# Optimization experiments

Measured on AMD Instinct MI355X. Metric: run time of the kernel, lower is better.

Reference implementation:

```python
import jax, jax.numpy as jnp
import numpy as np

N = 8192   # supervoxels in current scan (queries: mean_features / ori_coords)
M = 8192   # surrounding supervoxels (keys: sur_sv_feature / sur_sv_coords)
C = 96     # feature channels
OUT = 20   # semantic classes
LG = 2048  # number of labeled supervoxels


def _pairwise_l2(x, y):
    # squared euclidean distances [n, m], clamped at 0 like torch.clamp(d, 0, inf)
    xn = jnp.sum(x * x, axis=1)[:, None]
    yn = jnp.sum(y * y, axis=1)[None, :]
    d = xn + yn - 2.0 * (x @ y.T)
    return jnp.maximum(d, 0.0)


def _cosine_distance(x1, x2, eps=1e-8):
    w1 = jnp.linalg.norm(x1, axis=1, keepdims=True)
    w2 = jnp.linalg.norm(x2, axis=1, keepdims=True)
    return 1.0 - (x1 @ x2.T) / jnp.maximum(w1 * w2.T, eps)


def setup_inputs() -> dict:
    key = jax.random.key(0)
    ks = jax.random.split(key, 8)
    sur_sv_feature = 0.05 * jax.random.normal(ks[0], (M, C), jnp.float32)
    sur_sv_coords = 0.3 * jax.random.normal(ks[1], (M, 3), jnp.float32)
    gt_idx = jax.random.randint(ks[2], (M,), 0, OUT)
    sur_sv_gt = jnp.eye(OUT, dtype=jnp.float32)[gt_idx]
    sv_prob = jax.random.normal(ks[3], (N, OUT), jnp.float32)
    mean_features = 0.05 * jax.random.normal(ks[4], (N, C), jnp.float32)
    ori_coords = 0.3 * jax.random.normal(ks[5], (N, 3), jnp.float32)
    # two near-identity invertible 4x4 pose matrices
    posses = jnp.eye(4, dtype=jnp.float32)[None, :, :] + 0.02 * jax.random.normal(ks[6], (2, 4, 4), jnp.float32)
    ran_mask = jax.random.randint(ks[7], (M,), 0, 20).astype(jnp.int32)  # torch.randint(20, ...)
    return dict(sur_sv_feature=sur_sv_feature, sur_sv_coords=sur_sv_coords,
                sur_sv_gt=sur_sv_gt, sv_prob=sv_prob, mean_features=mean_features,
                ori_coords=ori_coords, posses=posses, ran_mask=ran_mask, lg=LG)


def reference(sur_sv_feature, sur_sv_coords, sur_sv_gt, sv_prob,
              mean_features, ori_coords, posses, ran_mask, lg):
    # branch: rev=1, idx=0, sf=None
    sv_prob_sm = jax.nn.softmax(sv_prob, axis=1)
    ori_coords_in = ori_coords
    # alginment: diff = inv(posses[1]) @ posses[0]; homogeneous transform
    diff = jnp.linalg.inv(posses[1]) @ posses[0]
    homog = jnp.concatenate([sur_sv_coords,
                             jnp.ones((sur_sv_coords.shape[0], 1), sur_sv_coords.dtype)], axis=1)
    al_sur_sv_coords = (homog @ diff.T)[:, :3]

    feat_dist_cos = _cosine_distance(mean_features, sur_sv_feature)          # [N, M]
    coords_dist = _pairwise_l2(ori_coords_in, al_sur_sv_coords) / 0.25       # / 0.5**2
    sim = (1.0 + feat_dist_cos - jnp.exp(-0.5 * coords_dist)).T              # [M, N]
    sm_index = jnp.argmin(sim, axis=1)                                       # [M] nearest query per key

    onehot = sur_sv_gt
    mid_feat = mean_features[sm_index]       # [M, C]
    mid_coord = ori_coords_in[sm_index]      # [M, 3]

    upd = jnp.argmax(onehot, axis=1) < 9
    upd = upd.at[:lg].set(True)
    upd = jnp.logical_or(upd, ran_mask == 1)                                 # random refresh mask

    # masked (instead of gathered) weighted label propagation: zeroed columns
    # contribute nothing to either numerator or denominator -> same math as
    # index-selecting the update columns.
    fd = _pairwise_l2(mean_features, mid_feat)                               # [N, M]
    cd = _pairwise_l2(ori_coords_in, mid_coord) / 0.25
    dist_matric = jnp.exp(-0.5 * cd / 0.25 - 0.5 * fd / 0.09) * upd[None, :].astype(fd.dtype)
    uw = (dist_matric @ onehot) / (jnp.sum(dist_matric, axis=1, keepdims=True) + 1e-16)

    sv_prob_updated = 0.5 * sv_prob_sm + 0.5 * uw

    # re-inject labeled gt where the propagated prob agrees enough
    tmpx = jnp.argmax(onehot[:lg], axis=1)                                   # [lg]
    idx_lg = sm_index[:lg]
    vals = sv_prob_updated[idx_lg, tmpx]
    tmp = vals > 0.1
    tmp = jnp.where(jnp.any(tmp), tmp, vals > 0.0)                           # fallback threshold
    new_rows = jnp.where(tmp[:, None], onehot[:lg], sv_prob_updated[idx_lg])
    sv_prob_updated = sv_prob_updated.at[idx_lg].set(new_rows)

    maxv = jnp.max(sv_prob_updated, axis=1)
    trust9 = maxv >= 0.9
    trust = jnp.where(jnp.any(trust9), trust9, maxv >= 0.85)                 # [N] bool mask (padded form of torch.nonzero)
    pre = jnp.eye(OUT, dtype=sv_prob_updated.dtype)[jnp.argmax(sv_prob_updated, axis=1)]

    m = trust[:, None].astype(mean_features.dtype)
    return (trust, mean_features * m, ori_coords * m, pre * m,
            uw, sv_prob_updated, sm_index)
```

## Files before the change

kernel.cpp:

```cpp
#include <hip/hip_runtime.h>
#include <math.h>

#define N 8192
#define M 8192
#define C 96
#define OUT 20
#define LG 2048

#define KP2 192
#define NSPA 4
#define NSPB 4

typedef _Float16 h8 __attribute__((ext_vector_type(8)));
typedef float    f4 __attribute__((ext_vector_type(4)));

__device__ __forceinline__ void gl_lds16(const h8* g, h8* l) {
    __builtin_amdgcn_global_load_lds(
        (const __attribute__((address_space(1))) unsigned int*)g,
        (__attribute__((address_space(3))) unsigned int*)l,
        16, 0, 0);
}

__device__ __forceinline__ size_t tsm24(int row, int slot) {
    return ((size_t)(row >> 7) * 24 + slot) * 128 + (row & 127);
}

constexpr size_t OFF_DIFF  = 0;
constexpr size_t OFF_AL    = 256;
constexpr size_t OFF_UPDF  = OFF_AL    + (size_t)M*3*4;
constexpr size_t OFF_GTC   = OFF_UPDF  + (size_t)M*4;
constexpr size_t OFF_SMI   = OFF_GTC   + (size_t)M*4;
constexpr size_t OFF_PERM  = OFF_SMI   + (size_t)M*4;
constexpr size_t OFF_AP    = OFF_PERM  + (size_t)M*4;
constexpr size_t OFF_BQ    = OFF_AP    + (size_t)M*KP2*2;
constexpr size_t OFF_MFP   = OFF_BQ    + (size_t)N*KP2*2;
constexpr size_t OFF_MIDQ  = OFF_MFP   + (size_t)N*KP2*2;
constexpr size_t OFF_PAV   = OFF_MIDQ  + (size_t)(M+256)*KP2*2;
constexpr size_t OFF_PAI   = OFF_PAV   + (size_t)NSPA*M*4;
constexpr size_t OFF_PB    = OFF_PAI   + (size_t)NSPA*M*4;
constexpr size_t OFF_VALS  = OFF_PB    + (size_t)NSPB*N*OUT*4;
constexpr size_t OFF_POS   = OFF_VALS  + (size_t)LG*4;
constexpr size_t OFF_MAXV  = OFF_POS   + (size_t)N*4;
constexpr size_t OFF_AMAX  = OFF_MAXV  + (size_t)N*4;
constexpr size_t OFF_FLAGS = OFF_AMAX  + (size_t)N*4;
constexpr size_t OFF_CNT   = OFF_FLAGS + 256;
constexpr size_t OFF_META  = OFF_CNT   + 256;
constexpr size_t OFF_NQ4   = OFF_META  + 256;
constexpr size_t OFF_SIDEQ = OFF_NQ4   + (size_t)N*16;
constexpr size_t OFF_SIDEC = OFF_SIDEQ + (size_t)(M+256)*16;

__global__ void k_diff(const float* __restrict__ posses, float* __restrict__ diff) {
    if (threadIdx.x != 0 || blockIdx.x != 0) return;
    float a[4][8];
    for (int i = 0; i < 4; i++)
        for (int j = 0; j < 4; j++) {
            a[i][j]     = posses[16 + i*4 + j];
            a[i][4 + j] = (i == j) ? 1.f : 0.f;
        }
    for (int col = 0; col < 4; col++) {
        int piv = col; float mx = fabsf(a[col][col]);
        for (int r = col + 1; r < 4; r++) {
            float v = fabsf(a[r][col]);
            if (v > mx) { mx = v; piv = r; }
        }
        if (piv != col)
            for (int j = 0; j < 8; j++) { float t = a[col][j]; a[col][j] = a[piv][j]; a[piv][j] = t; }
        float inv = 1.0f / a[col][col];
        for (int j = 0; j < 8; j++) a[col][j] *= inv;
        for (int r = 0; r < 4; r++) {
            if (r == col) continue;
            float f = a[r][col];
            for (int j = 0; j < 8; j++) a[r][j] -= f * a[col][j];
        }
    }
    for (int i = 0; i < 4; i++)
        for (int j = 0; j < 4; j++) {
            float s = 0.f;
            for (int k = 0; k < 4; k++) s += a[i][4 + k] * posses[k*4 + j];
            diff[i*4 + j] = s;
        }
}

__global__ void k_prep_m(const float* __restrict__ ssf, const float* __restrict__ scoords,
                         const float* __restrict__ gt, const int* __restrict__ ran_mask,
                         const float* __restrict__ diff,
                         float* __restrict__ al, _Float16* __restrict__ aP,
                         float* __restrict__ updf, int* __restrict__ gtcls,
                         int* __restrict__ cnt) {
    __shared__ int hcnt[OUT];
    const int tt = threadIdx.x;
    if (tt < OUT) hcnt[tt] = 0;
    __syncthreads();
    const int m = blockIdx.x * 32 + (tt >> 1);
    const int h = tt & 1;
    {
        const float4* r4 = (const float4*)(ssf + (size_t)m * C);
        float4 row[12]; float s = 0.f;
        #pragma unroll
        for (int c = 0; c < 12; c++) {
            float4 v = r4[h*12 + c];
            row[c] = v;
            s += v.x*v.x + v.y*v.y + v.z*v.z + v.w*v.w;
        }
        s += __shfl_xor(s, 1, 64);
        float scale = 256.0f / sqrtf(s);
        h8* dst = (h8*)aP;
        #pragma unroll
        for (int qq = 0; qq < 6; qq++) {
            int q = h*6 + qq;
            float4 u = row[2*qq], v = row[2*qq+1];
            float xs[8] = {u.x,u.y,u.z,u.w,v.x,v.y,v.z,v.w};
            h8 hi, lo;
            #pragma unroll
            for (int e = 0; e < 8; e++) {
                float xv = xs[e] * scale;
                _Float16 hh = (_Float16)xv;
                hi[e] = hh;
                lo[e] = (_Float16)(xv - (float)hh);
            }
            dst[tsm24(m, q)]      = hi;
            dst[tsm24(m, 12 + q)] = lo;
        }
        if (h == 0) {
            float x = scoords[m*3], y = scoords[m*3+1], z = scoords[m*3+2];
            #pragma unroll
            for (int j = 0; j < 3; j++)
                al[m*3 + j] = diff[j*4+0]*x + diff[j*4+1]*y + diff[j*4+2]*z + diff[j*4+3];
            int best = 0; float bv = gt[(size_t)m*OUT];
            #pragma unroll
            for (int k = 1; k < OUT; k++) {
                float v = gt[(size_t)m*OUT + k];
                if (v > bv) { bv = v; best = k; }
            }
            gtcls[m] = best;
            bool upd = (best < 9 || m < LG || ran_mask[m] == 1);
            updf[m] = upd ? 1.f : 0.f;
            if (upd) atomicAdd(&hcnt[best], 1);
        }
    }
    __syncthreads();
    if (tt < OUT) atomicAdd(&cnt[tt], hcnt[tt]);
}

__global__ void k_prep_n(const float* __restrict__ mf, const float* __restrict__ ori,
                         _Float16* __restrict__ bQ, _Float16* __restrict__ mfP,
                         float4* __restrict__ nq4) {
    const int tt = threadIdx.x;
    const int n = blockIdx.x * 32 + (tt >> 1);
    const int h = tt & 1;
    const float4* r4 = (const float4*)(mf + (size_t)n * C);
    float4 row[12]; float s = 0.f;
    #pragma unroll
    for (int c = 0; c < 12; c++) {
        float4 v = r4[h*12 + c];
        row[c] = v;
        s += v.x*v.x + v.y*v.y + v.z*v.z + v.w*v.w;
    }
    s += __shfl_xor(s, 1, 64);
    if (h == 0) {
        float4 o;
        o.x = ori[n*3]; o.y = ori[n*3+1]; o.z = ori[n*3+2]; o.w = s;
        nq4[n] = o;
    }
    float scn = 256.0f / sqrtf(s);
    h8* dB = (h8*)bQ;
    h8* dF = (h8*)mfP;
    #pragma unroll
    for (int qq = 0; qq < 6; qq++) {
        int q = h*6 + qq;
        float4 u = row[2*qq], v = row[2*qq+1];
        float xs[8] = {u.x,u.y,u.z,u.w,v.x,v.y,v.z,v.w};
        h8 hiN, loN, hiF, loF;
        #pragma unroll
        for (int e = 0; e < 8; e++) {
            float xn = xs[e] * scn;
            _Float16 hn = (_Float16)xn;
            hiN[e] = hn; loN[e] = (_Float16)(xn - (float)hn);
            float xf = xs[e] * 256.0f;
            _Float16 hf = (_Float16)xf;
            hiF[e] = hf; loF[e] = (_Float16)(xf - (float)hf);
        }
        dB[tsm24(n, q)]    = hiN;
        dB[tsm24(n, 12+q)] = loN;
        dF[tsm24(n, q)]    = hiF;
        dF[tsm24(n, 12+q)] = loF;
    }
}

__global__ __launch_bounds__(1024, 1) void k_argmin(
        const _Float16* __restrict__ aP, const _Float16* __restrict__ bQ,
        const float* __restrict__ al, const float4* __restrict__ nq4,
        float* __restrict__ pav, int* __restrict__ pai) {
    __shared__ h8 sA[24*128];
    __shared__ h8 sB[2*24*128];
    __shared__ float xv[4*128];
    __shared__ int   xi[4*128];
    __shared__ float4 sMs[128];
    const int t = threadIdx.x;
    const int wave = t >> 6, lane = t & 63;
    const int col = lane & 15, quad = lane >> 4;
    const int wm = wave >> 2, wn = wave & 3;
    const int m0 = blockIdx.x * 128;
    const int sp = blockIdx.y;

    {
        const h8* gA = (const h8*)aP + (size_t)blockIdx.x * 3072;
        #pragma unroll
        for (int q = 0; q < 3; q++) gl_lds16(gA + q*1024 + t, sA + q*1024 + t);
    }
    if (t < 128) {
        float ax = al[(m0+t)*3+0], ay = al[(m0+t)*3+1], az = al[(m0+t)*3+2];
        sMs[t] = (float4){4.0f*ax, 4.0f*ay, 4.0f*az, -2.0f*(ax*ax+ay*ay+az*az)};
    }
    float best[8]; int bidx[8];
    #pragma unroll
    for (int e = 0; e < 8; e++) { best[e] = 3.4e38f; bidx[e] = 0; }

    const h8* gB = (const h8*)bQ;
    f4 acc[2][4];
    for (int u = 0; u < 32/NSPA; u++) {
        const int tile = sp + u*NSPA;
        __syncthreads();
        {
            const h8* g = gB + (size_t)(2*tile) * 3072;
            #pragma unroll
            for (int q = 0; q < 6; q++) gl_lds16(g + q*1024 + t, sB + q*1024 + t);
        }
        __syncthreads();
        #pragma unroll
        for (int i = 0; i < 2; i++)
            #pragma unroll
            for (int j = 0; j < 4; j++) acc[i][j] = (f4){0.f,0.f,0.f,0.f};

        #pragma unroll
        for (int ks = 0; ks < 3; ks++) {
            const int hs = ks*4 + quad;
            h8 ah[2], alo[2], bh[4], blo[4];
            #pragma unroll
            for (int i = 0; i < 2; i++) {
                int ml = wm*32 + i*16 + col;
                ah[i]  = sA[hs*128 + ml];
                alo[i] = sA[(12+hs)*128 + ml];
            }
            #pragma unroll
            for (int j = 0; j < 4; j++) {
                int r = wn*64 + j*16 + col;
                int tb = (r >> 7) * 3072, rl = r & 127;
                bh[j]  = sB[tb + hs*128 + rl];
                blo[j] = sB[tb + (12+hs)*128 + rl];
            }
            #pragma unroll
            for (int i = 0; i < 2; i++)
                #pragma unroll
                for (int j = 0; j < 4; j++) {
                    acc[i][j] = __builtin_amdgcn_mfma_f32_16x16x32_f16(ah[i],  bh[j],  acc[i][j], 0, 0, 0);
                    acc[i][j] = __builtin_amdgcn_mfma_f32_16x16x32_f16(ah[i],  blo[j], acc[i][j], 0, 0, 0);
                    acc[i][j] = __builtin_amdgcn_mfma_f32_16x16x32_f16(alo[i], bh[j],  acc[i][j], 0, 0, 0);
                }
        }
        const int n0t = tile * 256;
        float4 o4[4]; float bn[4]; int nidx[4];
        #pragma unroll
        for (int j = 0; j < 4; j++) {
            nidx[j] = n0t + wn*64 + j*16 + col;
            o4[j] = nq4[nidx[j]];
            bn[j] = -2.0f*(o4[j].x*o4[j].x + o4[j].y*o4[j].y + o4[j].z*o4[j].z);
        }
        #pragma unroll
        for (int e = 0; e < 8; e++) {
            int ml = wm*32 + (e>>2)*16 + quad*4 + (e&3);
            float4 sm = sMs[ml];
            #pragma unroll
            for (int j = 0; j < 4; j++) {
                float dot = acc[e>>2][j][e&3];
                float c = sm.w + bn[j];
                c = fmaf(sm.z, o4[j].z, c);
                c = fmaf(sm.y, o4[j].y, c);
                c = fmaf(sm.x, o4[j].x, c);
                float sim = fmaf(dot, -(1.0f/65536.0f), 2.0f) - __expf(c);
                if (sim < best[e]) { best[e] = sim; bidx[e] = nidx[j]; }
            }
        }
    }
    #pragma unroll
    for (int e = 0; e < 8; e++) {
        float bv = best[e]; int bi = bidx[e];
        #pragma unroll
        for (int d = 1; d < 16; d <<= 1) {
            float ov = __shfl_xor(bv, d, 64);
            int   oi = __shfl_xor(bi, d, 64);
            if (ov < bv || (ov == bv && oi < bi)) { bv = ov; bi = oi; }
        }
        best[e] = bv; bidx[e] = bi;
    }
    if (col == 0) {
        #pragma unroll
        for (int e = 0; e < 8; e++) {
            int ml = wm*32 + (e>>2)*16 + quad*4 + (e&3);
            xv[wn*128 + ml] = best[e];
            xi[wn*128 + ml] = bidx[e];
        }
    }
    __syncthreads();
    if (t < 128) {
        float bv = xv[t]; int bi = xi[t];
        #pragma unroll
        for (int w = 1; w < 4; w++) {
            float v = xv[w*128 + t]; int i2 = xi[w*128 + t];
            if (v < bv || (v == bv && i2 < bi)) { bv = v; bi = i2; }
        }
        pav[(size_t)sp * M + m0 + t] = bv;
        pai[(size_t)sp * M + m0 + t] = bi;
    }
}

__global__ void k_argmin_reduce(const float* __restrict__ pav, const int* __restrict__ pai,
                                int* __restrict__ smi, float* __restrict__ out_smi) {
    int m = blockIdx.x * 256 + threadIdx.x;
    if (m >= M) return;
    float best = 3.4e38f; int bidx = 0;
    for (int sp = 0; sp < NSPA; sp++) {
        float v = pav[(size_t)sp * M + m];
        int   i = pai[(size_t)sp * M + m];
        if (v < best || (v == best && i < bidx)) { best = v; bidx = i; }
    }
    smi[m] = bidx;
    out_smi[m] = (float)bidx;
}

__global__ void k_scan(const int* __restrict__ cnt, int* __restrict__ meta) {
    if (threadIdx.x != 0 || blockIdx.x != 0) return;
    int run = 0;
    for (int k = 0; k < OUT; k++) { meta[2 + k] = run; run += cnt[k]; }
    meta[0] = run;
    meta[1] = (run + 255) / 256;
}

__global__ void k_permute(const int* __restrict__ gtcls, const float* __restrict__ updf,
                          int* __restrict__ meta, int* __restrict__ perm) {
    int m = blockIdx.x * 256 + threadIdx.x;
    if (m >= M) return;
    if (updf[m] == 0.f) return;
    int pos = atomicAdd(&meta[2 + gtcls[m]], 1);
    perm[pos] = m;
}

__global__ void k_gather_sorted(const int* __restrict__ meta, const int* __restrict__ perm,
                                const int* __restrict__ smi, const int* __restrict__ gtcls,
                                const _Float16* __restrict__ mfP, const float4* __restrict__ nq4,
                                _Float16* __restrict__ midQ,
                                float4* __restrict__ sideQ, int* __restrict__ sideC) {
    int tid = blockIdx.x * 256 + threadIdx.x;
    int rr = tid / 24;
    int q  = tid - rr * 24;
    int mact = meta[0];
    int mpad = meta[1] * 256;
    if (rr >= mpad) return;
    h8* dst = (h8*)midQ;
    if (rr < mact) {
        int m = perm[rr];
        int s = smi[m];
        dst[tsm24(rr, q)] = ((const h8*)mfP)[tsm24(s, q)];
        if (q == 0) {
            float4 o = nq4[s];
            float4 sq;
            sq.x = o.w;
            sq.y = o.x; sq.z = o.y; sq.w = o.z;
            sideQ[rr] = sq;
            sideC[rr] = gtcls[m];
        }
    } else {
        dst[tsm24(rr, q)] = (h8)(_Float16)0.f;
        if (q == 0) {
            sideQ[rr] = (float4){1e9f, 0.f, 0.f, 0.f};
            sideC[rr] = 0;
        }
    }
}

__global__ __launch_bounds__(1024, 1) void k_uw(
        const _Float16* __restrict__ mfP, const _Float16* __restrict__ midQ,
        const float4* __restrict__ nq4,
        const float4* __restrict__ sideQ, const int* __restrict__ sideC,
        const int* __restrict__ meta, float* __restrict__ pb) {
    __shared__ h8 sN[24*128];
    __shared__ h8 sB[2*24*128];
    __shared__ float bins[128*21];
    __shared__ float4 sSa[128];
    __shared__ float  sSb[128];
    const int t = threadIdx.x;
    const int wave = t >> 6, lane = t & 63;
    const int col = lane & 15, quad = lane >> 4;
    const int wm = wave >> 2, wn = wave & 3;
    const int n0 = blockIdx.x * 128;
    const int sp = blockIdx.y;
    const int nmac = meta[1];

    {
        const h8* gN = (const h8*)mfP + (size_t)blockIdx.x * 3072;
        #pragma unroll
        for (int q = 0; q < 3; q++) gl_lds16(gN + q*1024 + t, sN + q*1024 + t);
    }
    if (t < 128) {
        float4 q = nq4[n0 + t];
        sSa[t] = (float4){q.x, q.y, q.z, -8.0f*(q.x*q.x + q.y*q.y + q.z*q.z)};
        sSb[t] = q.w;
    }
    for (int i = t; i < 128*21; i += 1024) bins[i] = 0.f;

    const h8* gB = (const h8*)midQ;
    f4 acc[2][4];
    for (int mt = sp; mt < nmac; mt += NSPB) {
        const int mb = mt * 256;
        __syncthreads();
        {
            const h8* g = gB + (size_t)(2*mt) * 3072;
            #pragma unroll
            for (int q = 0; q < 6; q++) gl_lds16(g + q*1024 + t, sB + q*1024 + t);
        }
        __syncthreads();
        #pragma unroll
        for (int i = 0; i < 2; i++)
            #pragma unroll
            for (int j = 0; j < 4; j++) acc[i][j] = (f4){0.f,0.f,0.f,0.f};

        #pragma unroll
        for (int ks = 0; ks < 3; ks++) {
            const int hs = ks*4 + quad;
            h8 ah[2], alo[2], bh[4], blo[4];
            #pragma unroll
            for (int i = 0; i < 2; i++) {
                int ml = wm*32 + i*16 + col;
                ah[i]  = sN[hs*128 + ml];
                alo[i] = sN[(12+hs)*128 + ml];
            }
            #pragma unroll
            for (int j = 0; j < 4; j++) {
                int r = wn*64 + j*16 + col;
                int tb = (r >> 7) * 3072, rl = r & 127;
                bh[j]  = sB[tb + hs*128 + rl];
                blo[j] = sB[tb + (12+hs)*128 + rl];
            }
            #pragma unroll
            for (int i = 0; i < 2; i++)
                #pragma unroll
                for (int j = 0; j < 4; j++) {
                    acc[i][j] = __builtin_amdgcn_mfma_f32_16x16x32_f16(ah[i],  bh[j],  acc[i][j], 0, 0, 0);
                    acc[i][j] = __builtin_amdgcn_mfma_f32_16x16x32_f16(ah[i],  blo[j], acc[i][j], 0, 0, 0);
                    acc[i][j] = __builtin_amdgcn_mfma_f32_16x16x32_f16(alo[i], bh[j],  acc[i][j], 0, 0, 0);
                }
        }
        {
            float m2[4], mx16[4], my16[4], mz16[4], bm[4]; int pc[4];
            #pragma unroll
            for (int j = 0; j < 4; j++) {
                int mm = mb + wn*64 + j*16 + col;
                float4 sq = sideQ[mm];
                m2[j] = sq.x;
                mx16[j] = 16.0f*sq.y; my16[j] = 16.0f*sq.z; mz16[j] = 16.0f*sq.w;
                bm[j] = -8.0f*(sq.y*sq.y + sq.z*sq.z + sq.w*sq.w);
                pc[j] = sideC[mm];
            }
            int seg0 = sideC[mb + wn*64];
            int seg1 = sideC[mb + wn*64 + 63];
            if (seg0 == seg1) {
                #pragma unroll
                for (int e = 0; e < 8; e++) {
                    int nl = wm*32 + (e>>2)*16 + quad*4 + (e&3);
                    float4 sa = sSa[nl];
                    float nn = sSb[nl];
                    float rs = 0.f;
                    #pragma unroll
                    for (int j = 0; j < 4; j++) {
                        float dot = acc[e>>2][j][e&3];
                        float tt = fmaf(dot, -2.0f*(1.0f/65536.0f), nn + m2[j]);
                        float fd = fmaxf(tt, 0.0f);
                        float c = sa.w + bm[j];
                        c = fmaf(sa.z, mz16[j], c);
                        c = fmaf(sa.y, my16[j], c);
                        c = fmaf(sa.x, mx16[j], c);
                        rs += __expf(fmaf(fd, -(0.5f/0.09f), c));
                    }
                    rs += __shfl_xor(rs, 1, 64);
                    rs += __shfl_xor(rs, 2, 64);
                    rs += __shfl_xor(rs, 4, 64);
                    rs += __shfl_xor(rs, 8, 64);
                    if (col == 0) atomicAdd(&bins[nl*21 + seg0], rs);
                }
            } else {
                #pragma unroll
                for (int e = 0; e < 8; e++) {
                    int nl = wm*32 + (e>>2)*16 + quad*4 + (e&3);
                    float4 sa = sSa[nl];
                    float nn = sSb[nl];
                    float cur = 0.f; int cc = -1;
                    #pragma unroll
                    for (int j = 0; j < 4; j++) {
                        float dot = acc[e>>2][j][e&3];
                        float tt = fmaf(dot, -2.0f*(1.0f/65536.0f), nn + m2[j]);
                        float fd = fmaxf(tt, 0.0f);
                        float c = sa.w + bm[j];
                        c = fmaf(sa.z, mz16[j], c);
                        c = fmaf(sa.y, my16[j], c);
                        c = fmaf(sa.x, mx16[j], c);
                        float w = __expf(fmaf(fd, -(0.5f/0.09f), c));
                        if (pc[j] != cc) {
                            if (cc >= 0) atomicAdd(&bins[nl*21 + cc], cur);
                            cc = pc[j]; cur = 0.f;
                        }
                        cur += w;
                    }
                    if (cc >= 0) atomicAdd(&bins[nl*21 + cc], cur);
                }
            }
        }
    }
    __syncthreads();
    for (int i = t; i < 128*OUT; i += 1024) {
        int loc = i / OUT, k = i - loc*OUT;
        pb[((size_t)sp*N + n0 + loc)*OUT + k] = bins[loc*21 + k];
    }
}

__global__ void k_uw_final(const float* __restrict__ pb, const float* __restrict__ svp,
                           float* __restrict__ out_uw, float* __restrict__ out_spu) {
    int n = blockIdx.x * 256 + threadIdx.x;
    if (n >= N) return;
    float s[OUT];
    #pragma unroll
    for (int k = 0; k < OUT; k++) s[k] = 0.f;
    for (int sp = 0; sp < NSPB; sp++) {
        size_t base = ((size_t)sp * N + n) * OUT;
        #pragma unroll
        for (int k = 0; k < OUT; k++) s[k] += pb[base + k];
    }
    float tot = 0.f;
    #pragma unroll
    for (int k = 0; k < OUT; k++) tot += s[k];
    float rden = 1.0f / (tot + 1e-16f);
    float p[OUT]; float mx = -3.4e38f;
    #pragma unroll
    for (int k = 0; k < OUT; k++) { p[k] = svp[(size_t)n*OUT + k]; mx = fmaxf(mx, p[k]); }
    float es = 0.f;
    #pragma unroll
    for (int k = 0; k < OUT; k++) { p[k] = __expf(p[k] - mx); es += p[k]; }
    float res = 1.0f / es;
    #pragma unroll
    for (int k = 0; k < OUT; k++) {
        float uw = s[k] * rden;
        out_uw[(size_t)n*OUT + k] = uw;
        out_spu[(size_t)n*OUT + k] = 0.5f * (p[k] * res) + 0.5f * uw;
    }
}

__global__ void k_scatter_pre(const int* __restrict__ smi, const int* __restrict__ gtcls,
                              const float* __restrict__ spu, float* __restrict__ vals,
                              int* __restrict__ pos, int* __restrict__ flags) {
    int i = blockIdx.x * 256 + threadIdx.x;
    if (i >= LG) return;
    int idx = smi[i];
    float v = spu[(size_t)idx*OUT + gtcls[i]];
    vals[i] = v;
    if (v > 0.1f) atomicOr(&flags[0], 1);
    atomicMax(&pos[idx], i);
}

__global__ void k_scatter_apply(const int* __restrict__ smi, const int* __restrict__ gtcls,
                                const float* __restrict__ vals, const int* __restrict__ pos,
                                const int* __restrict__ flags, float* __restrict__ spu) {
    int i = blockIdx.x * 256 + threadIdx.x;
    if (i >= LG) return;
    int idx = smi[i];
    if (pos[idx] != i) return;
    float v = vals[i];
    bool tmp = flags[0] ? (v > 0.1f) : (v > 0.0f);
    if (!tmp) return;
    int cls = gtcls[i];
    #pragma unroll
    for (int k = 0; k < OUT; k++) spu[(size_t)idx*OUT + k] = (k == cls) ? 1.0f : 0.0f;
}

__global__ void k_trust_pre(const float* __restrict__ spu, float* __restrict__ maxv,
                            int* __restrict__ amax, int* __restrict__ flags) {
    int n = blockIdx.x * 256 + threadIdx.x;
    if (n >= N) return;
    float best = spu[(size_t)n*OUT]; int bi = 0;
    #pragma unroll
    for (int k = 1; k < OUT; k++) {
        float v = spu[(size_t)n*OUT + k];
        if (v > best) { best = v; bi = k; }
    }
    maxv[n] = best; amax[n] = bi;
    if (best >= 0.9f) atomicOr(&flags[1], 1);
}

__global__ void k_finalize(const float* __restrict__ mf, const float* __restrict__ ori,
                           const float* __restrict__ maxv, const int* __restrict__ amax,
                           const int* __restrict__ flags,
                           float* __restrict__ out_trust, float* __restrict__ out_mf,
                           float* __restrict__ out_ori, float* __restrict__ out_pre) {
    int n = blockIdx.x * 256 + threadIdx.x;
    if (n >= N) return;
    float mv = maxv[n];
    bool tr = flags[1] ? (mv >= 0.9f) : (mv >= 0.85f);
    float m = tr ? 1.f : 0.f;
    out_trust[n] = m;
    const float4* src = (const float4*)(mf + (size_t)n * C);
    float4* dst = (float4*)(out_mf + (size_t)n * C);
    #pragma unroll
    for (int c = 0; c < 24; c++) {
        float4 v = src[c];
        v.x *= m; v.y *= m; v.z *= m; v.w *= m;
        dst[c] = v;
    }
    out_ori[n*3]   = ori[n*3]   * m;
    out_ori[n*3+1] = ori[n*3+1] * m;
    out_ori[n*3+2] = ori[n*3+2] * m;
    int bi = amax[n];
    #pragma unroll
    for (int k = 0; k < OUT; k++) out_pre[(size_t)n*OUT + k] = (k == bi) ? m : 0.f;
}

extern "C" void kernel_launch(void* const* d_in, const int* in_sizes, int n_in,
                              void* d_out, int out_size, void* d_ws, size_t ws_size,
                              hipStream_t stream) {
    (void)in_sizes; (void)n_in; (void)out_size; (void)ws_size;
    const float* ssf     = (const float*)d_in[0];
    const float* scoords = (const float*)d_in[1];
    const float* gt      = (const float*)d_in[2];
    const float* svp     = (const float*)d_in[3];
    const float* mf      = (const float*)d_in[4];
    const float* ori     = (const float*)d_in[5];
    const float* posses  = (const float*)d_in[6];
    const int*   ran     = (const int*)d_in[7];

    float* out = (float*)d_out;
    float* out_trust = out;
    float* out_mf    = out_trust + N;
    float* out_ori   = out_mf + (size_t)N*C;
    float* out_pre   = out_ori + (size_t)N*3;
    float* out_uw    = out_pre + (size_t)N*OUT;
    float* out_spu   = out_uw  + (size_t)N*OUT;
    float* out_smi   = out_spu + (size_t)N*OUT;

    char* ws = (char*)d_ws;
    float*     w_diff  = (float*)(ws + OFF_DIFF);
    float*     w_al    = (float*)(ws + OFF_AL);
    float*     w_updf  = (float*)(ws + OFF_UPDF);
    int*       w_gtc   = (int*)(ws + OFF_GTC);
    int*       w_smi   = (int*)(ws + OFF_SMI);
    int*       w_perm  = (int*)(ws + OFF_PERM);
    _Float16*  w_aP    = (_Float16*)(ws + OFF_AP);
    _Float16*  w_bQ    = (_Float16*)(ws + OFF_BQ);
    _Float16*  w_mfP   = (_Float16*)(ws + OFF_MFP);
    _Float16*  w_midQ  = (_Float16*)(ws + OFF_MIDQ);
    float*     w_pav   = (float*)(ws + OFF_PAV);
    int*       w_pai   = (int*)(ws + OFF_PAI);
    float*     w_pb    = (float*)(ws + OFF_PB);
    float*     w_vals  = (float*)(ws + OFF_VALS);
    int*       w_pos   = (int*)(ws + OFF_POS);
    float*     w_maxv  = (float*)(ws + OFF_MAXV);
    int*       w_amax  = (int*)(ws + OFF_AMAX);
    int*       w_flags = (int*)(ws + OFF_FLAGS);
    int*       w_cnt   = (int*)(ws + OFF_CNT);
    int*       w_meta  = (int*)(ws + OFF_META);
    float4*    w_nq4   = (float4*)(ws + OFF_NQ4);
    float4*    w_sideQ = (float4*)(ws + OFF_SIDEQ);
    int*       w_sideC = (int*)(ws + OFF_SIDEC);

    hipMemsetAsync(w_pos, 0xFF, (size_t)N*4, stream);
    hipMemsetAsync(w_flags, 0, 8, stream);
    hipMemsetAsync(w_cnt, 0, OUT*4, stream);

    k_diff<<<1, 64, 0, stream>>>(posses, w_diff);
    k_prep_m<<<M/32, 64, 0, stream>>>(ssf, scoords, gt, ran, w_diff,
                                      w_al, w_aP, w_updf, w_gtc, w_cnt);
    k_prep_n<<<N/32, 64, 0, stream>>>(mf, ori, w_bQ, w_mfP, w_nq4);
    k_argmin<<<dim3(M/128, NSPA), 1024, 0, stream>>>(w_aP, w_bQ, w_al, w_nq4, w_pav, w_pai);
    k_argmin_reduce<<<M/256, 256, 0, stream>>>(w_pav, w_pai, w_smi, out_smi);
    k_scan<<<1, 64, 0, stream>>>(w_cnt, w_meta);
    k_permute<<<M/256, 256, 0, stream>>>(w_gtc, w_updf, w_meta, w_perm);
    k_gather_sorted<<<((M+256)*24)/256, 256, 0, stream>>>(w_meta, w_perm, w_smi, w_gtc,
                                                          w_mfP, w_nq4,
                                                          w_midQ, w_sideQ, w_sideC);
    k_uw<<<dim3(N/128, NSPB), 1024, 0, stream>>>(w_mfP, w_midQ, w_nq4,
                                                 w_sideQ, w_sideC, w_meta, w_pb);
    k_uw_final<<<N/256, 256, 0, stream>>>(w_pb, svp, out_uw, out_spu);
    k_scatter_pre<<<LG/256, 256, 0, stream>>>(w_smi, w_gtc, out_spu, w_vals, w_pos, w_flags);
    k_scatter_apply<<<LG/256, 256, 0, stream>>>(w_smi, w_gtc, w_vals, w_pos, w_flags, out_spu);
    k_trust_pre<<<N/256, 256, 0, stream>>>(out_spu, w_maxv, w_amax, w_flags);
    k_finalize<<<N/256, 256, 0, stream>>>(mf, ori, w_maxv, w_amax, w_flags,
                                          out_trust, out_mf, out_ori, out_pre);
}
```

Baseline: 253.9 us.

## Double-buffer key tiles, drop low-half B operand, use shuffle-reduced class bins

The key matrix (midH) is now stored as the high fp16 half only, which halves gather and LDS traffic and removes one of the three MFMAs per split-precision product. Key tiles are prefetched into a second LDS buffer while the current one is being computed, so there is one barrier per iteration instead of two. The per-lane running class-segment atomics are replaced by a loop over classes with a cross-lane shuffle reduction and a single atomic per class. Dropping the low correction term on the key side lowers precision of the feature dot product, and the loop over classes may cost extra work when a tile spans several classes.

Result: faster. 228.3 us (-10.1%).

```diff
diff --git a/kernel.cpp b/kernel.cpp
--- a/kernel.cpp
+++ b/kernel.cpp
@@ -34,8 +34,8 @@
 constexpr size_t OFF_AP    = OFF_PERM  + (size_t)M*4;
 constexpr size_t OFF_BQ    = OFF_AP    + (size_t)M*KP2*2;
 constexpr size_t OFF_MFP   = OFF_BQ    + (size_t)N*KP2*2;
-constexpr size_t OFF_MIDQ  = OFF_MFP   + (size_t)N*KP2*2;
-constexpr size_t OFF_PAV   = OFF_MIDQ  + (size_t)(M+256)*KP2*2;
+constexpr size_t OFF_MIDH  = OFF_MFP   + (size_t)N*KP2*2;
+constexpr size_t OFF_PAV   = OFF_MIDH  + (size_t)(M+256)*192;
 constexpr size_t OFF_PAI   = OFF_PAV   + (size_t)NSPA*M*4;
 constexpr size_t OFF_PB    = OFF_PAI   + (size_t)NSPA*M*4;
 constexpr size_t OFF_VALS  = OFF_PB    + (size_t)NSPB*N*OUT*4;
@@ -348,19 +348,20 @@
 __global__ void k_gather_sorted(const int* __restrict__ meta, const int* __restrict__ perm,
                                 const int* __restrict__ smi, const int* __restrict__ gtcls,
                                 const _Float16* __restrict__ mfP, const float4* __restrict__ nq4,
-                                _Float16* __restrict__ midQ,
+                                _Float16* __restrict__ midH,
                                 float4* __restrict__ sideQ, int* __restrict__ sideC) {
     int tid = blockIdx.x * 256 + threadIdx.x;
-    int rr = tid / 24;
-    int q  = tid - rr * 24;
+    int rr = tid / 12;
+    int q  = tid - rr * 12;
     int mact = meta[0];
     int mpad = meta[1] * 256;
     if (rr >= mpad) return;
-    h8* dst = (h8*)midQ;
+    h8* dst = (h8*)midH;
+    size_t didx = ((size_t)(rr >> 7) * 12 + q) * 128 + (rr & 127);
     if (rr < mact) {
         int m = perm[rr];
         int s = smi[m];
-        dst[tsm24(rr, q)] = ((const h8*)mfP)[tsm24(s, q)];
+        dst[didx] = ((const h8*)mfP)[tsm24(s, q)];
         if (q == 0) {
             float4 o = nq4[s];
             float4 sq;
@@ -370,7 +371,7 @@
             sideC[rr] = gtcls[m];
         }
     } else {
-        dst[tsm24(rr, q)] = (h8)(_Float16)0.f;
+        dst[didx] = (h8)(_Float16)0.f;
         if (q == 0) {
             sideQ[rr] = (float4){1e9f, 0.f, 0.f, 0.f};
             sideC[rr] = 0;
@@ -379,12 +380,12 @@
 }
 
 __global__ __launch_bounds__(1024, 1) void k_uw(
-        const _Float16* __restrict__ mfP, const _Float16* __restrict__ midQ,
+        const _Float16* __restrict__ mfP, const _Float16* __restrict__ midH,
         const float4* __restrict__ nq4,
         const float4* __restrict__ sideQ, const int* __restrict__ sideC,
         const int* __restrict__ meta, float* __restrict__ pb) {
     __shared__ h8 sN[24*128];
-    __shared__ h8 sB[2*24*128];
+    __shared__ h8 sB[2][2*12*128];
     __shared__ float bins[128*21];
     __shared__ float4 sSa[128];
     __shared__ float  sSb[128];
@@ -400,6 +401,11 @@
         const h8* gN = (const h8*)mfP + (size_t)blockIdx.x * 3072;
         #pragma unroll
         for (int q = 0; q < 3; q++) gl_lds16(gN + q*1024 + t, sN + q*1024 + t);
+        if (sp < nmac) {
+            const h8* g = (const h8*)midH + (size_t)(2*sp) * 1536;
+            #pragma unroll
+            for (int q = 0; q < 3; q++) gl_lds16(g + q*1024 + t, sB[0] + q*1024 + t);
+        }
     }
     if (t < 128) {
         float4 q = nq4[n0 + t];
@@ -408,26 +414,27 @@
     }
     for (int i = t; i < 128*21; i += 1024) bins[i] = 0.f;
 
-    const h8* gB = (const h8*)midQ;
+    __syncthreads();
+
+    int cur = 0;
     f4 acc[2][4];
     for (int mt = sp; mt < nmac; mt += NSPB) {
         const int mb = mt * 256;
-        __syncthreads();
-        {
-            const h8* g = gB + (size_t)(2*mt) * 3072;
-            #pragma unroll
-            for (int q = 0; q < 6; q++) gl_lds16(g + q*1024 + t, sB + q*1024 + t);
-        }
-        __syncthreads();
+        if (mt + NSPB < nmac) {
+            const h8* g = (const h8*)midH + (size_t)(2*(mt + NSPB)) * 1536;
+            #pragma unroll
+            for (int q = 0; q < 3; q++) gl_lds16(g + q*1024 + t, sB[cur^1] + q*1024 + t);
+        }
         #pragma unroll
         for (int i = 0; i < 2; i++)
             #pragma unroll
             for (int j = 0; j < 4; j++) acc[i][j] = (f4){0.f,0.f,0.f,0.f};
 
+        const h8* sBc = sB[cur];
         #pragma unroll
         for (int ks = 0; ks < 3; ks++) {
             const int hs = ks*4 + quad;
-            h8 ah[2], alo[2], bh[4], blo[4];
+            h8 ah[2], alo[2], bh[4];
             #pragma unroll
             for (int i = 0; i < 2; i++) {
                 int ml = wm*32 + i*16 + col;
@@ -437,17 +444,15 @@
             #pragma unroll
             for (int j = 0; j < 4; j++) {
                 int r = wn*64 + j*16 + col;
-                int tb = (r >> 7) * 3072, rl = r & 127;
-                bh[j]  = sB[tb + hs*128 + rl];
-                blo[j] = sB[tb + (12+hs)*128 + rl];
+                int tb = (r >> 7) * 1536, rl = r & 127;
+                bh[j]  = sBc[tb + hs*128 + rl];
             }
             #pragma unroll
             for (int i = 0; i < 2; i++)
                 #pragma unroll
                 for (int j = 0; j < 4; j++) {
-                    acc[i][j] = __builtin_amdgcn_mfma_f32_16x16x32_f16(ah[i],  bh[j],  acc[i][j], 0, 0, 0);
-                    acc[i][j] = __builtin_amdgcn_mfma_f32_16x16x32_f16(ah[i],  blo[j], acc[i][j], 0, 0, 0);
-                    acc[i][j] = __builtin_amdgcn_mfma_f32_16x16x32_f16(alo[i], bh[j],  acc[i][j], 0, 0, 0);
+                    acc[i][j] = __builtin_amdgcn_mfma_f32_16x16x32_f16(ah[i],  bh[j], acc[i][j], 0, 0, 0);
+                    acc[i][j] = __builtin_amdgcn_mfma_f32_16x16x32_f16(alo[i], bh[j], acc[i][j], 0, 0, 0);
                 }
         }
         {
@@ -493,7 +498,7 @@
                     int nl = wm*32 + (e>>2)*16 + quad*4 + (e&3);
                     float4 sa = sSa[nl];
                     float nn = sSb[nl];
-                    float cur = 0.f; int cc = -1;
+                    float w[4];
                     #pragma unroll
                     for (int j = 0; j < 4; j++) {
                         float dot = acc[e>>2][j][e&3];
@@ -503,17 +508,23 @@
                         c = fmaf(sa.z, mz16[j], c);
                         c = fmaf(sa.y, my16[j], c);
                         c = fmaf(sa.x, mx16[j], c);
-                        float w = __expf(fmaf(fd, -(0.5f/0.09f), c));
-                        if (pc[j] != cc) {
-                            if (cc >= 0) atomicAdd(&bins[nl*21 + cc], cur);
-                            cc = pc[j]; cur = 0.f;
-                        }
-                        cur += w;
+                        w[j] = __expf(fmaf(fd, -(0.5f/0.09f), c));
                     }
-                    if (cc >= 0) atomicAdd(&bins[nl*21 + cc], cur);
+                    for (int cc = seg0; cc <= seg1; cc++) {
+                        float rs = 0.f;
+                        #pragma unroll
+                        for (int j = 0; j < 4; j++) rs += (pc[j] == cc) ? w[j] : 0.f;
+                        rs += __shfl_xor(rs, 1, 64);
+                        rs += __shfl_xor(rs, 2, 64);
+                        rs += __shfl_xor(rs, 4, 64);
+                        rs += __shfl_xor(rs, 8, 64);
+                        if (col == 0) atomicAdd(&bins[nl*21 + cc], rs);
+                    }
                 }
             }
         }
+        __syncthreads();
+        cur ^= 1;
     }
     __syncthreads();
     for (int i = t; i < 128*OUT; i += 1024) {
@@ -653,7 +664,7 @@
     _Float16*  w_aP    = (_Float16*)(ws + OFF_AP);
     _Float16*  w_bQ    = (_Float16*)(ws + OFF_BQ);
     _Float16*  w_mfP   = (_Float16*)(ws + OFF_MFP);
-    _Float16*  w_midQ  = (_Float16*)(ws + OFF_MIDQ);
+    _Float16*  w_midH  = (_Float16*)(ws + OFF_MIDH);
     float*     w_pav   = (float*)(ws + OFF_PAV);
     int*       w_pai   = (int*)(ws + OFF_PAI);
     float*     w_pb    = (float*)(ws + OFF_PB);
@@ -680,10 +691,10 @@
     k_argmin_reduce<<<M/256, 256, 0, stream>>>(w_pav, w_pai, w_smi, out_smi);
     k_scan<<<1, 64, 0, stream>>>(w_cnt, w_meta);
     k_permute<<<M/256, 256, 0, stream>>>(w_gtc, w_updf, w_meta, w_perm);
-    k_gather_sorted<<<((M+256)*24)/256, 256, 0, stream>>>(w_meta, w_perm, w_smi, w_gtc,
+    k_gather_sorted<<<((M+256)*12)/256, 256, 0, stream>>>(w_meta, w_perm, w_smi, w_gtc,
                                                           w_mfP, w_nq4,
-                                                          w_midQ, w_sideQ, w_sideC);
-    k_uw<<<dim3(N/128, NSPB), 1024, 0, stream>>>(w_mfP, w_midQ, w_nq4,
+                                                          w_midH, w_sideQ, w_sideC);
+    k_uw<<<dim3(N/128, NSPB), 1024, 0, stream>>>(w_mfP, w_midH, w_nq4,
                                                  w_sideQ, w_sideC, w_meta, w_pb);
     k_uw_final<<<N/256, 256, 0, stream>>>(w_pb, svp, out_uw, out_spu);
     k_scatter_pre<<<LG/256, 256, 0, stream>>>(w_smi, w_gtc, out_spu, w_vals, w_pos, w_flags);
```

## Double-buffer B tiles with async LDS prefetch and fold log2e into exp2

Applied to the files above, without the earlier changes.

In both the argmin and uw kernels, the 256-column B tile is halved to 128 columns, so it fits a ping-pong pair of LDS buffers. The next tile is prefetched via global_load_lds while the current one is computed, and each iteration needs one barrier instead of two. Exponentials become exp2f with LOG2E folded into the precomputed coefficients. The mixed-segment path in k_uw now reduces per class with wave shuffles plus one atomic per lane group, instead of per-lane atomics. Halving the tile gives each wave less MFMA work per barrier, and correctness depends on the async LDS writes having finished before the end-of-iteration barrier.

Result: no change. 249.1 us (-1.9%).

```diff
diff --git a/kernel.cpp b/kernel.cpp
--- a/kernel.cpp
+++ b/kernel.cpp
@@ -10,6 +10,7 @@
 #define KP2 192
 #define NSPA 4
 #define NSPB 4
+#define LOG2E 1.4426950408889634f
 
 typedef _Float16 h8 __attribute__((ext_vector_type(8)));
 typedef float    f4 __attribute__((ext_vector_type(4)));
@@ -192,7 +193,7 @@
         const float* __restrict__ al, const float4* __restrict__ nq4,
         float* __restrict__ pav, int* __restrict__ pai) {
     __shared__ h8 sA[24*128];
-    __shared__ h8 sB[2*24*128];
+    __shared__ h8 sB[2][24*128];
     __shared__ float xv[4*128];
     __shared__ int   xi[4*128];
     __shared__ float4 sMs[128];
@@ -207,35 +208,41 @@
         const h8* gA = (const h8*)aP + (size_t)blockIdx.x * 3072;
         #pragma unroll
         for (int q = 0; q < 3; q++) gl_lds16(gA + q*1024 + t, sA + q*1024 + t);
+        const h8* g = (const h8*)bQ + (size_t)sp * 3072;
+        #pragma unroll
+        for (int q = 0; q < 3; q++) gl_lds16(g + q*1024 + t, sB[0] + q*1024 + t);
     }
     if (t < 128) {
         float ax = al[(m0+t)*3+0], ay = al[(m0+t)*3+1], az = al[(m0+t)*3+2];
-        sMs[t] = (float4){4.0f*ax, 4.0f*ay, 4.0f*az, -2.0f*(ax*ax+ay*ay+az*az)};
+        sMs[t] = (float4){4.0f*LOG2E*ax, 4.0f*LOG2E*ay, 4.0f*LOG2E*az,
+                          -2.0f*LOG2E*(ax*ax+ay*ay+az*az)};
     }
     float best[8]; int bidx[8];
     #pragma unroll
     for (int e = 0; e < 8; e++) { best[e] = 3.4e38f; bidx[e] = 0; }
 
-    const h8* gB = (const h8*)bQ;
-    f4 acc[2][4];
-    for (int u = 0; u < 32/NSPA; u++) {
+    __syncthreads();
+
+    const int NT = (N/128) / NSPA;
+    int cur = 0;
+    f4 acc[2][2];
+    for (int u = 0; u < NT; u++) {
         const int tile = sp + u*NSPA;
-        __syncthreads();
-        {
-            const h8* g = gB + (size_t)(2*tile) * 3072;
-            #pragma unroll
-            for (int q = 0; q < 6; q++) gl_lds16(g + q*1024 + t, sB + q*1024 + t);
-        }
-        __syncthreads();
+        if (u + 1 < NT) {
+            const h8* g = (const h8*)bQ + (size_t)(sp + (u+1)*NSPA) * 3072;
+            #pragma unroll
+            for (int q = 0; q < 3; q++) gl_lds16(g + q*1024 + t, sB[cur^1] + q*1024 + t);
+        }
         #pragma unroll
         for (int i = 0; i < 2; i++)
             #pragma unroll
-            for (int j = 0; j < 4; j++) acc[i][j] = (f4){0.f,0.f,0.f,0.f};
-
+            for (int j = 0; j < 2; j++) acc[i][j] = (f4){0.f,0.f,0.f,0.f};
+
+        const h8* sBc = sB[cur];
         #pragma unroll
         for (int ks = 0; ks < 3; ks++) {
             const int hs = ks*4 + quad;
-            h8 ah[2], alo[2], bh[4], blo[4];
+            h8 ah[2], alo[2], bh[2], blo[2];
             #pragma unroll
             for (int i = 0; i < 2; i++) {
                 int ml = wm*32 + i*16 + col;
@@ -243,44 +250,45 @@
                 alo[i] = sA[(12+hs)*128 + ml];
             }
             #pragma unroll
-            for (int j = 0; j < 4; j++) {
-                int r = wn*64 + j*16 + col;
-                int tb = (r >> 7) * 3072, rl = r & 127;
-                bh[j]  = sB[tb + hs*128 + rl];
-                blo[j] = sB[tb + (12+hs)*128 + rl];
+            for (int j = 0; j < 2; j++) {
+                int r = wn*32 + j*16 + col;
+                bh[j]  = sBc[hs*128 + r];
+                blo[j] = sBc[(12+hs)*128 + r];
             }
             #pragma unroll
             for (int i = 0; i < 2; i++)
                 #pragma unroll
-                for (int j = 0; j < 4; j++) {
+                for (int j = 0; j < 2; j++) {
                     acc[i][j] = __builtin_amdgcn_mfma_f32_16x16x32_f16(ah[i],  bh[j],  acc[i][j], 0, 0, 0);
                     acc[i][j] = __builtin_amdgcn_mfma_f32_16x16x32_f16(ah[i],  blo[j], acc[i][j], 0, 0, 0);
                     acc[i][j] = __builtin_amdgcn_mfma_f32_16x16x32_f16(alo[i], bh[j],  acc[i][j], 0, 0, 0);
                 }
         }
-        const int n0t = tile * 256;
-        float4 o4[4]; float bn[4]; int nidx[4];
-        #pragma unroll
-        for (int j = 0; j < 4; j++) {
-            nidx[j] = n0t + wn*64 + j*16 + col;
+        const int n0t = tile * 128;
+        float4 o4[2]; float bn[2]; int nidx[2];
+        #pragma unroll
+        for (int j = 0; j < 2; j++) {
+            nidx[j] = n0t + wn*32 + j*16 + col;
             o4[j] = nq4[nidx[j]];
-            bn[j] = -2.0f*(o4[j].x*o4[j].x + o4[j].y*o4[j].y + o4[j].z*o4[j].z);
+            bn[j] = -2.0f*LOG2E*(o4[j].x*o4[j].x + o4[j].y*o4[j].y + o4[j].z*o4[j].z);
         }
         #pragma unroll
         for (int e = 0; e < 8; e++) {
             int ml = wm*32 + (e>>2)*16 + quad*4 + (e&3);
             float4 sm = sMs[ml];
             #pragma unroll
-            for (int j = 0; j < 4; j++) {
+            for (int j = 0; j < 2; j++) {
                 float dot = acc[e>>2][j][e&3];
                 float c = sm.w + bn[j];
                 c = fmaf(sm.z, o4[j].z, c);
                 c = fmaf(sm.y, o4[j].y, c);
                 c = fmaf(sm.x, o4[j].x, c);
-                float sim = fmaf(dot, -(1.0f/65536.0f), 2.0f) - __expf(c);
+                float sim = fmaf(dot, -(1.0f/65536.0f), 2.0f) - exp2f(c);
                 if (sim < best[e]) { best[e] = sim; bidx[e] = nidx[j]; }
             }
         }
+        __syncthreads();
+        cur ^= 1;
     }
     #pragma unroll
     for (int e = 0; e < 8; e++) {
@@ -384,7 +392,7 @@
         const float4* __restrict__ sideQ, const int* __restrict__ sideC,
         const int* __restrict__ meta, float* __restrict__ pb) {
     __shared__ h8 sN[24*128];
-    __shared__ h8 sB[2*24*128];
+    __shared__ h8 sB[2][24*128];
     __shared__ float bins[128*21];
     __shared__ float4 sSa[128];
     __shared__ float  sSb[128];
@@ -394,40 +402,46 @@
     const int wm = wave >> 2, wn = wave & 3;
     const int n0 = blockIdx.x * 128;
     const int sp = blockIdx.y;
-    const int nmac = meta[1];
+    const int nmac2 = meta[1] * 2;
 
     {
         const h8* gN = (const h8*)mfP + (size_t)blockIdx.x * 3072;
         #pragma unroll
         for (int q = 0; q < 3; q++) gl_lds16(gN + q*1024 + t, sN + q*1024 + t);
+        if (sp < nmac2) {
+            const h8* g = (const h8*)midQ + (size_t)sp * 3072;
+            #pragma unroll
+            for (int q = 0; q < 3; q++) gl_lds16(g + q*1024 + t, sB[0] + q*1024 + t);
+        }
     }
     if (t < 128) {
         float4 q = nq4[n0 + t];
-        sSa[t] = (float4){q.x, q.y, q.z, -8.0f*(q.x*q.x + q.y*q.y + q.z*q.z)};
+        sSa[t] = (float4){q.x, q.y, q.z, -8.0f*LOG2E*(q.x*q.x + q.y*q.y + q.z*q.z)};
         sSb[t] = q.w;
     }
     for (int i = t; i < 128*21; i += 1024) bins[i] = 0.f;
 
-    const h8* gB = (const h8*)midQ;
-    f4 acc[2][4];
-    for (int mt = sp; mt < nmac; mt += NSPB) {
-        const int mb = mt * 256;
-        __syncthreads();
-        {
-            const h8* g = gB + (size_t)(2*mt) * 3072;
-            #pragma unroll
-            for (int q = 0; q < 6; q++) gl_lds16(g + q*1024 + t, sB + q*1024 + t);
-        }
-        __syncthreads();
+    __syncthreads();
+
+    int cur = 0;
+    f4 acc[2][2];
+    for (int mt = sp; mt < nmac2; mt += NSPB) {
+        const int mb = mt * 128;
+        if (mt + NSPB < nmac2) {
+            const h8* g = (const h8*)midQ + (size_t)(mt + NSPB) * 3072;
+            #pragma unroll
+            for (int q = 0; q < 3; q++) gl_lds16(g + q*1024 + t, sB[cur^1] + q*1024 + t);
+        }
         #pragma unroll
         for (int i = 0; i < 2; i++)
             #pragma unroll
-            for (int j = 0; j < 4; j++) acc[i][j] = (f4){0.f,0.f,0.f,0.f};
-
+            for (int j = 0; j < 2; j++) acc[i][j] = (f4){0.f,0.f,0.f,0.f};
+
+        const h8* sBc = sB[cur];
         #pragma unroll
         for (int ks = 0; ks < 3; ks++) {
             const int hs = ks*4 + quad;
-            h8 ah[2], alo[2], bh[4], blo[4];
+            h8 ah[2], alo[2], bh[2], blo[2];
             #pragma unroll
             for (int i = 0; i < 2; i++) {
                 int ml = wm*32 + i*16 + col;
@@ -435,34 +449,33 @@
                 alo[i] = sN[(12+hs)*128 + ml];
             }
             #pragma unroll
-            for (int j = 0; j < 4; j++) {
-                int r = wn*64 + j*16 + col;
-                int tb = (r >> 7) * 3072, rl = r & 127;
-                bh[j]  = sB[tb + hs*128 + rl];
-                blo[j] = sB[tb + (12+hs)*128 + rl];
+            for (int j = 0; j < 2; j++) {
+                int r = wn*32 + j*16 + col;
+                bh[j]  = sBc[hs*128 + r];
+                blo[j] = sBc[(12+hs)*128 + r];
             }
             #pragma unroll
             for (int i = 0; i < 2; i++)
                 #pragma unroll
-                for (int j = 0; j < 4; j++) {
+                for (int j = 0; j < 2; j++) {
                     acc[i][j] = __builtin_amdgcn_mfma_f32_16x16x32_f16(ah[i],  bh[j],  acc[i][j], 0, 0, 0);
                     acc[i][j] = __builtin_amdgcn_mfma_f32_16x16x32_f16(ah[i],  blo[j], acc[i][j], 0, 0, 0);
                     acc[i][j] = __builtin_amdgcn_mfma_f32_16x16x32_f16(alo[i], bh[j],  acc[i][j], 0, 0, 0);
                 }
         }
         {
-            float m2[4], mx16[4], my16[4], mz16[4], bm[4]; int pc[4];
-            #pragma unroll
-            for (int j = 0; j < 4; j++) {
-                int mm = mb + wn*64 + j*16 + col;
+            float m2[2], mx16[2], my16[2], mz16[2], bm[2]; int pc[2];
+            #pragma unroll
+            for (int j = 0; j < 2; j++) {
+                int mm = mb + wn*32 + j*16 + col;
                 float4 sq = sideQ[mm];
                 m2[j] = sq.x;
-                mx16[j] = 16.0f*sq.y; my16[j] = 16.0f*sq.z; mz16[j] = 16.0f*sq.w;
-                bm[j] = -8.0f*(sq.y*sq.y + sq.z*sq.z + sq.w*sq.w);
+                mx16[j] = 16.0f*LOG2E*sq.y; my16[j] = 16.0f*LOG2E*sq.z; mz16[j] = 16.0f*LOG2E*sq.w;
+                bm[j] = -8.0f*LOG2E*(sq.y*sq.y + sq.z*sq.z + sq.w*sq.w);
                 pc[j] = sideC[mm];
             }
-            int seg0 = sideC[mb + wn*64];
-            int seg1 = sideC[mb + wn*64 + 63];
+            int seg0 = sideC[mb + wn*32];
+            int seg1 = sideC[mb + wn*32 + 31];
             if (seg0 == seg1) {
                 #pragma unroll
                 for (int e = 0; e < 8; e++) {
@@ -471,7 +484,7 @@
                     float nn = sSb[nl];
                     float rs = 0.f;
                     #pragma unroll
-                    for (int j = 0; j < 4; j++) {
+                    for (int j = 0; j < 2; j++) {
                         float dot = acc[e>>2][j][e&3];
                         float tt = fmaf(dot, -2.0f*(1.0f/65536.0f), nn + m2[j]);
                         float fd = fmaxf(tt, 0.0f);
@@ -479,7 +492,7 @@
                         c = fmaf(sa.z, mz16[j], c);
                         c = fmaf(sa.y, my16[j], c);
                         c = fmaf(sa.x, mx16[j], c);
-                        rs += __expf(fmaf(fd, -(0.5f/0.09f), c));
+                        rs += exp2f(fmaf(fd, -(0.5f/0.09f)*LOG2E, c));
                     }
                     rs += __shfl_xor(rs, 1, 64);
                     rs += __shfl_xor(rs, 2, 64);
@@ -493,9 +506,9 @@
                     int nl = wm*32 + (e>>2)*16 + quad*4 + (e&3);
                     float4 sa = sSa[nl];
                     float nn = sSb[nl];
-                    float cur = 0.f; int cc = -1;
+                    float w[2];
                     #pragma unroll
-                    for (int j = 0; j < 4; j++) {
+                    for (int j = 0; j < 2; j++) {
                         float dot = acc[e>>2][j][e&3];
                         float tt = fmaf(dot, -2.0f*(1.0f/65536.0f), nn + m2[j]);
                         float fd = fmaxf(tt, 0.0f);
@@ -503,17 +516,23 @@
                         c = fmaf(sa.z, mz16[j], c);
                         c = fmaf(sa.y, my16[j], c);
                         c = fmaf(sa.x, mx16[j], c);
-                        float w = __expf(fmaf(fd, -(0.5f/0.09f), c));
-                        if (pc[j] != cc) {
-                            if (cc >= 0) atomicAdd(&bins[nl*21 + cc], cur);
-                            cc = pc[j]; cur = 0.f;
-                        }
-                        cur += w;
+                        w[j] = exp2f(fmaf(fd, -(0.5f/0.09f)*LOG2E, c));
                     }
-                    if (cc >= 0) atomicAdd(&bins[nl*21 + cc], cur);
+                    for (int cc = seg0; cc <= seg1; cc++) {
+                        float rs = 0.f;
+                        #pragma unroll
+                        for (int j = 0; j < 2; j++) rs += (pc[j] == cc) ? w[j] : 0.f;
+                        rs += __shfl_xor(rs, 1, 64);
+                        rs += __shfl_xor(rs, 2, 64);
+                        rs += __shfl_xor(rs, 4, 64);
+                        rs += __shfl_xor(rs, 8, 64);
+                        if (col == 0) atomicAdd(&bins[nl*21 + cc], rs);
+                    }
                 }
             }
         }
+        __syncthreads();
+        cur ^= 1;
     }
     __syncthreads();
     for (int i = t; i < 128*OUT; i += 1024) {
```
